# Kernel optimization log

Measured on AMD Instinct MI355X. Metric: run time of the kernel, lower is better.

The kernel has to match this reference:

```python
import jax, jax.numpy as jnp
import numpy as np

HIDDEN = 4096
NUM_BLOCKS = 8
BLOCK = HIDDEN // NUM_BLOCKS  # 512


def setup_inputs() -> dict:
    key = jax.random.key(0)
    k1, k2, k3, k4 = jax.random.split(key, 4)
    return {
        "weight": jax.random.normal(k1, (HIDDEN, HIDDEN), dtype=jnp.float32) * 0.02,
        "bias": jax.random.normal(k2, (HIDDEN,), dtype=jnp.float32) * 0.02,
        "x": jax.random.normal(k3, (4, 2048, HIDDEN), dtype=jnp.float32),
        "proj_R": jax.random.normal(k4, (NUM_BLOCKS, BLOCK, BLOCK), dtype=jnp.float32) * 0.02,
        "layer_idx": 0,
    }


def _cayley_batch(A):
    # Q = (I - S) @ inv(I + S + 1e-6*I), S = 0.5*(A - A^T), batched over blocks
    r = A.shape[-1]
    I = jnp.eye(r, dtype=A.dtype)
    S = 0.5 * (A - jnp.swapaxes(A, -2, -1))
    Minv = jnp.linalg.inv(I + S + 1e-6 * I)
    return jnp.einsum('bij,bjk->bik', I - S, Minv)


def reference(weight, bias, x, proj_R, layer_idx):
    Q = _cayley_batch(proj_R)                     # [nb, bs, bs], orthogonal blocks
    nb, bs, _ = Q.shape
    # block_diag(Q) @ weight == batched block-row matmul (off-diagonal blocks are zero)
    Wb = weight.reshape(nb, bs, weight.shape[1])  # [nb, bs, in]
    filt = jnp.einsum('bij,bjk->bik', Q, Wb).reshape(nb * bs, weight.shape[1])
    # F.linear(x, filt, bias)
    return jnp.einsum('bsi,oi->bso', x, filt) + bias
```

## Files before the change

### kernel.cpp

```cpp
#include <hip/hip_runtime.h>

typedef unsigned short u16;
typedef __attribute__((ext_vector_type(8))) short bf16x8;
typedef __attribute__((ext_vector_type(4))) float f32x4;
typedef __attribute__((ext_vector_type(8))) unsigned short u16x8;
typedef __attribute__((ext_vector_type(4))) unsigned short u16x4;

__device__ __forceinline__ u16 f2bf(float f){
  unsigned int u = __builtin_bit_cast(unsigned int, f);
  u += 0x7FFFu + ((u >> 16) & 1u);
  return (u16)(u >> 16);
}
__device__ __forceinline__ float bf2f(u16 h){
  unsigned int u = ((unsigned int)h) << 16;
  return __builtin_bit_cast(float, u);
}

__device__ __forceinline__ void load16(const u16* g, u16* s){
  __builtin_amdgcn_global_load_lds((const __attribute__((address_space(1))) unsigned int*)g,
                                   (__attribute__((address_space(3))) unsigned int*)s,
                                   16, 0, 0);
}

__global__ __launch_bounds__(256) void build_s(const float* __restrict__ R, u16* __restrict__ Sbf,
                                               u16* __restrict__ Dbf){
  int idx = blockIdx.x * 256 + threadIdx.x;
  int b = idx >> 18;
  int i = (idx >> 9) & 511;
  int j = idx & 511;
  float a  = R[idx];
  float at = R[(b << 18) + (j << 9) + i];
  float s = 0.5f * (a - at);
  Sbf[idx] = f2bf(s);
  Dbf[idx] = f2bf((i == j ? 2.000003f : 0.0f) - 2.000001f * s);
}

__global__ __launch_bounds__(256) void conv_bf16(const float* __restrict__ src, u16* __restrict__ dst){
  size_t i = (size_t)blockIdx.x * 256 + threadIdx.x;
  const float4* s = (const float4*)src + i * 2;
  float4 v0 = s[0], v1 = s[1];
  u16x8 o = { f2bf(v0.x), f2bf(v0.y), f2bf(v0.z), f2bf(v0.w),
              f2bf(v1.x), f2bf(v1.y), f2bf(v1.z), f2bf(v1.w) };
  *(u16x8*)(dst + i * 8) = o;
}

__global__ __launch_bounds__(256) void transpose_w(const float* __restrict__ W, u16* __restrict__ Wt){
  const int b = blockIdx.z;
  const int i0 = blockIdx.x << 5;
  const int j0 = blockIdx.y << 5;
  __shared__ float tile[32][33];
  const int t = threadIdx.x;
  const int r = t >> 3, c = (t & 7) << 2;
  float4 v = *(const float4*)&W[(size_t)((b << 9) + j0 + r) * 4096 + i0 + c];
  tile[r][c+0] = v.x; tile[r][c+1] = v.y; tile[r][c+2] = v.z; tile[r][c+3] = v.w;
  __syncthreads();
  u16x4 o = { f2bf(tile[c+0][r]), f2bf(tile[c+1][r]), f2bf(tile[c+2][r]), f2bf(tile[c+3][r]) };
  *(u16x4*)&Wt[((size_t)b << 21) + (size_t)(i0 + r) * 512 + j0 + c] = o;
}

template<int EPI>
__global__ __launch_bounds__(256) void gemm_bt(const u16* __restrict__ A, const u16* __restrict__ B,
                                               void* __restrict__ Cout, const void* __restrict__ aux,
                                               void* __restrict__ aux2,
                                               int M, int N, int K){
  const int bz = blockIdx.z;
  const u16* Ab = A + (size_t)bz * M * K;
  const u16* Bb = B + (size_t)bz * N * K;
  const int m0 = blockIdx.y << 7, n0 = blockIdx.x << 7;
  __shared__ __align__(16) u16 As[4096];
  __shared__ __align__(16) u16 Bs[4096];
  const int t = threadIdx.x;
  const int w = t >> 6, l = t & 63;
  const int wr = w >> 1, wc = w & 1;
  const int kofs = (l & 3) << 3;
  const int rA = l >> 2;
  const int aRd = ((wr << 6) + (l & 15)) * 32 + ((l >> 4) << 3);
  const int bRd = ((wc << 6) + (l & 15)) * 32 + ((l >> 4) << 3);
  f32x4 acc[4][4] = {};
  for (int k0 = 0; k0 < K; k0 += 32){
#pragma unroll
    for (int j = 0; j < 2; ++j){
      int rowBase = ((w << 1) + j) << 4;
      load16(&Ab[(size_t)(m0 + rowBase + rA) * K + k0 + kofs], &As[((w << 1) + j) << 9]);
      load16(&Bb[(size_t)(n0 + rowBase + rA) * K + k0 + kofs], &Bs[((w << 1) + j) << 9]);
    }
    __syncthreads();
    bf16x8 aF[4], bF[4];
#pragma unroll
    for (int mf = 0; mf < 4; ++mf) aF[mf] = *(const bf16x8*)&As[aRd + (mf << 9)];
#pragma unroll
    for (int nf = 0; nf < 4; ++nf) bF[nf] = *(const bf16x8*)&Bs[bRd + (nf << 9)];
#pragma unroll
    for (int mf = 0; mf < 4; ++mf)
#pragma unroll
      for (int nf = 0; nf < 4; ++nf)
        acc[mf][nf] = __builtin_amdgcn_mfma_f32_16x16x32_bf16(aF[mf], bF[nf], acc[mf][nf], 0, 0, 0);
    __syncthreads();
  }
#pragma unroll
  for (int mf = 0; mf < 4; ++mf){
#pragma unroll
    for (int nf = 0; nf < 4; ++nf){
      const int col = n0 + (wc << 6) + (nf << 4) + (l & 15);
#pragma unroll
      for (int q = 0; q < 4; ++q){
        const int row = m0 + (wr << 6) + (mf << 4) + ((l >> 4) << 2) + q;
        float v = acc[mf][nf][q];
        size_t gi = ((size_t)bz * M + row) * N + col;
        size_t g2 = (((size_t)bz * M + row) << 10) + col;
        if (EPI == 3){
          ((u16*)Cout)[gi] = f2bf((row == col ? 2.0f : 0.0f) - v);
        } else if (EPI == 6){
          ((u16*)Cout)[gi] = f2bf(bf2f(((const u16*)aux)[gi]) + v);
        } else if (EPI == 7){
          u16 o = f2bf(v);
          ((u16*)Cout)[gi] = o;
          u16* d = (u16*)const_cast<void*>(aux);
          d[g2] = o;
          d[g2 + 512] = o;
        } else if (EPI == 9){
          ((u16*)Cout)[gi] = f2bf(v - (row == col ? 1.0f : 0.0f));
        } else if (EPI == 10){
          ((u16*)Cout)[gi] = f2bf((row == col ? 1.0f : 0.0f) - v);
        } else {
          float p = v + (row == col ? 1.000002f : 0.0f);
          u16 ph = f2bf(p);
          ((u16*)Cout)[g2] = ph;
          ((u16*)Cout)[g2 + 512] = f2bf(p - bf2f(ph));
          const float beta = 0.8264463f;
          u16 x1 = f2bf((row == col ? 2.0f * beta : 0.0f) - beta * beta * p);
          ((u16*)const_cast<void*>(aux))[gi] = x1;
          ((u16*)aux2)[g2] = x1;
          ((u16*)aux2)[g2 + 512] = x1;
        }
      }
    }
  }
}

template<int EPI>
__global__ __launch_bounds__(512, 2) void gemm256(const u16* __restrict__ A, const u16* __restrict__ B,
                                                  void* __restrict__ Cout, const float* __restrict__ aux,
                                                  int M, int N, int K){
  __shared__ __align__(16) char lds[131072];
  const int bz = blockIdx.z;
  const char* Ab = (const char*)(A + (size_t)bz * M * K);
  const char* Bb = (const char*)(B + (size_t)bz * N * K);
  const int NB = N >> 8;
  const int nwg = gridDim.x;
  const int bid = blockIdx.x;
  const int swzb = (bid & 7) * (nwg >> 3) + (bid >> 3);
  const int m0 = (swzb / NB) << 8;
  const int n0 = (swzb % NB) << 8;
  const int tid = threadIdx.x;
  const int w = tid >> 6, l = tid & 63;
  const int wm = w >> 2, wn = w & 3;
  const size_t Kb = (size_t)K << 1;
  const int NT = K >> 6;
  const int sRow = tid >> 3;
  const int sCol = ((tid & 7) << 4) ^ ((sRow & 7) << 4);
  const int sDst = tid << 4;
  const char* aS = Ab + (size_t)(m0 + sRow) * Kb + sCol;
  const char* bS = Bb + (size_t)(n0 + sRow) * Kb + sCol;
  const int lrow = (l & 15) << 7;
  const int kq0 = (((l >> 4) << 4)) ^ ((l & 7) << 4);
  const int aOff = (wm << 14) + lrow;
  const int bOff = 32768 + ((wn >> 1) << 14) + ((wn & 1) << 13) + lrow;

#define STAGE_H(isB, h, tt) { \
    const int _lo = (((tt) & 1) << 16) + ((isB) << 15) + ((h) << 14); \
    const char* _s = ((isB) ? bS : aS) + ((size_t)((h) << 7)) * Kb + ((size_t)(tt) << 7); \
    load16((const u16*)_s, (u16*)(lds + _lo + sDst)); \
    load16((const u16*)(_s + (Kb << 6)), (u16*)(lds + _lo + 8192 + sDst)); }

#define RD_A(bufb, UQ) \
  _Pragma("unroll") for (int i2 = 0; i2 < 4; ++i2){ \
    aF[i2][0] = *(const bf16x8*)(lds + (bufb) + aOff + ((UQ) << 13) + (i2 << 11) + kq0); \
    aF[i2][1] = *(const bf16x8*)(lds + (bufb) + aOff + ((UQ) << 13) + (i2 << 11) + (kq0 ^ 64)); }

#define RD_B(bufb, VQ) \
  _Pragma("unroll") for (int j2 = 0; j2 < 2; ++j2){ \
    bF[VQ][j2][0] = *(const bf16x8*)(lds + (bufb) + bOff + ((VQ) << 12) + (j2 << 11) + kq0); \
    bF[VQ][j2][1] = *(const bf16x8*)(lds + (bufb) + bOff + ((VQ) << 12) + (j2 << 11) + (kq0 ^ 64)); }

#define MFMA16(UQ, VQ) \
    _Pragma("unroll") for (int i2 = 0; i2 < 4; ++i2) \
      _Pragma("unroll") for (int j2 = 0; j2 < 2; ++j2){ \
        acc[(UQ)*4+i2][(VQ)*2+j2] = __builtin_amdgcn_mfma_f32_16x16x32_bf16(aF[i2][0], bF[VQ][j2][0], acc[(UQ)*4+i2][(VQ)*2+j2], 0, 0, 0); \
        acc[(UQ)*4+i2][(VQ)*2+j2] = __builtin_amdgcn_mfma_f32_16x16x32_bf16(aF[i2][1], bF[VQ][j2][1], acc[(UQ)*4+i2][(VQ)*2+j2], 0, 0, 0); }

#define BAR asm volatile("s_barrier" ::: "memory");
#define VM0 asm volatile("s_waitcnt vmcnt(0)" ::: "memory");

  bf16x8 aF[4][2], bF[2][2][2];
  f32x4 acc[8][4] = {};

  STAGE_H(0,0,0) STAGE_H(1,0,0) STAGE_H(0,1,0) STAGE_H(1,1,0)
  VM0 BAR

#define KTILE(t, bufb) { \
    RD_A(bufb, 0) RD_B(bufb, 0) \
    if ((t) + 1 < NT) { STAGE_H(0,0,(t)+1) STAGE_H(1,0,(t)+1) } \
    MFMA16(0,0) \
    RD_B(bufb, 1) \
    if ((t) + 1 < NT) { STAGE_H(0,1,(t)+1) STAGE_H(1,1,(t)+1) } \
    MFMA16(0,1) \
    RD_A(bufb, 1) \
    MFMA16(1,1) \
    MFMA16(1,0) \
    __builtin_amdgcn_sched_barrier(0); \
    VM0 BAR }

#pragma unroll 1
  for (int tp = 0; tp < NT; tp += 2){
    KTILE(tp, 0)
    KTILE(tp+1, 65536)
  }
#undef KTILE
#undef STAGE_H
#undef RD_A
#undef RD_B
#undef MFMA16
#undef BAR
#undef VM0

#pragma unroll
  for (int mf = 0; mf < 8; ++mf){
#pragma unroll
    for (int nf = 0; nf < 4; ++nf){
      const int col = n0 + (wn << 6) + (nf << 4) + (l & 15);
#pragma unroll
      for (int q = 0; q < 4; ++q){
        const int row = m0 + (wm << 7) + (mf << 4) + ((l >> 4) << 2) + q;
        float v = acc[mf][nf][q];
        if (EPI == 0){
          ((float*)Cout)[(size_t)row * N + col] = v + aux[col];
        } else {
          ((u16*)Cout)[((size_t)bz * M + row) * N + col] = f2bf(v);
        }
      }
    }
  }
}

extern "C" void kernel_launch(void* const* d_in, const int* in_sizes, int n_in,
                              void* d_out, int out_size, void* d_ws, size_t ws_size,
                              hipStream_t stream){
  const float* W    = (const float*)d_in[0];
  const float* bias = (const float*)d_in[1];
  const float* x    = (const float*)d_in[2];
  const float* R    = (const float*)d_in[3];
  (void)in_sizes; (void)n_in; (void)out_size; (void)ws_size;

  char* ws = (char*)d_ws;
  const size_t MiB = (size_t)1 << 20;
  u16*   Sbf  = (u16*)(ws + 0 * MiB);
  u16*   Dbf  = (u16*)(ws + 4 * MiB);
  u16*   X1   = (u16*)(ws + 16 * MiB);
  u16*   Ybf  = (u16*)(ws + 20 * MiB);
  u16*   X2   = (u16*)(ws + 24 * MiB);
  u16*   Phl  = (u16*)(ws + 28 * MiB);
  u16*   X2d  = (u16*)(ws + 36 * MiB);
  u16*   X1d  = (u16*)(ws + 44 * MiB);
  u16*   Rbf  = X1;
  u16*   X3   = Ybf;
  u16*   G    = Sbf;
  u16*   Wt   = (u16*)(ws + 8 * MiB);
  u16*   filt = (u16*)(ws + 64 * MiB);
  u16*   xbf  = (u16*)(ws + 0 * MiB);

  const dim3 gNS(4, 4, 8);

  build_s<<<8192, 256, 0, stream>>>(R, Sbf, Dbf);
  gemm_bt<11><<<gNS, 256, 0, stream>>>(Sbf, Sbf, Phl, X1, X1d, 512, 512, 512);
  gemm_bt<3><<<gNS, 256, 0, stream>>>(Phl, X1d, Ybf, nullptr, nullptr, 512, 512, 1024);
  gemm_bt<7><<<gNS, 256, 0, stream>>>(X1, Ybf, X2, X2d, nullptr, 512, 512, 512);
  gemm_bt<10><<<gNS, 256, 0, stream>>>(Phl, X2d, Rbf, nullptr, nullptr, 512, 512, 1024);
  gemm_bt<6><<<gNS, 256, 0, stream>>>(X2, Rbf, X3, X2, nullptr, 512, 512, 512);
  gemm_bt<9><<<gNS, 256, 0, stream>>>(Dbf, X3, G, nullptr, nullptr, 512, 512, 512);
  transpose_w<<<dim3(128, 16, 8), 256, 0, stream>>>(W, Wt);
  gemm256<2><<<dim3(32, 1, 8), 512, 0, stream>>>(G, Wt, (void*)filt, nullptr, 512, 4096, 512);
  conv_bf16<<<16384, 256, 0, stream>>>(x, xbf);
  gemm256<0><<<dim3(512, 1, 1), 512, 0, stream>>>(xbf, filt, d_out, bias, 8192, 4096, 4096);
}
```

Before: 410.5 us.

## Use 4-wave 256x256 GEMM blocks with 128x128 per-wave tiles

Moves the main GEMM kernel from 8 waves (512 threads) to 4 waves (256 threads) per 256x256 output tile, so each wave now computes a 128x128 sub-tile with an 8x8 grid of 16x16 MFMA accumulators. The interleaved half-stage prefetch and MFMA schedule is replaced by a simpler order: issue all next-tile global-to-LDS loads, read all fragments, then run two 64-MFMA groups. The aim is more fragment reuse per LDS read and fewer waves contending for LDS bandwidth. In exchange, register use per thread roughly doubles (256 accumulator floats plus 32 fragment vectors), which can lower occupancy or spill, and there are fewer waves available to hide latency.

```diff
diff --git a/kernel.cpp b/kernel.cpp
--- a/kernel.cpp
+++ b/kernel.cpp
@@ -139,7 +139,7 @@
 }
 
 template<int EPI>
-__global__ __launch_bounds__(512, 2) void gemm256(const u16* __restrict__ A, const u16* __restrict__ B,
+__global__ __launch_bounds__(256, 1) void gemm256(const u16* __restrict__ A, const u16* __restrict__ B,
                                                   void* __restrict__ Cout, const float* __restrict__ aux,
                                                   int M, int N, int K){
   __shared__ __align__(16) char lds[131072];
@@ -154,7 +154,7 @@
   const int n0 = (swzb % NB) << 8;
   const int tid = threadIdx.x;
   const int w = tid >> 6, l = tid & 63;
-  const int wm = w >> 2, wn = w & 3;
+  const int wm = w >> 1, wn = w & 1;
   const size_t Kb = (size_t)K << 1;
   const int NT = K >> 6;
   const int sRow = tid >> 3;
@@ -162,52 +162,42 @@
   const int sDst = tid << 4;
   const char* aS = Ab + (size_t)(m0 + sRow) * Kb + sCol;
   const char* bS = Bb + (size_t)(n0 + sRow) * Kb + sCol;
-  const int lrow = (l & 15) << 7;
   const int kq0 = (((l >> 4) << 4)) ^ ((l & 7) << 4);
-  const int aOff = (wm << 14) + lrow;
-  const int bOff = 32768 + ((wn >> 1) << 14) + ((wn & 1) << 13) + lrow;
-
-#define STAGE_H(isB, h, tt) { \
-    const int _lo = (((tt) & 1) << 16) + ((isB) << 15) + ((h) << 14); \
-    const char* _s = ((isB) ? bS : aS) + ((size_t)((h) << 7)) * Kb + ((size_t)(tt) << 7); \
-    load16((const u16*)_s, (u16*)(lds + _lo + sDst)); \
-    load16((const u16*)(_s + (Kb << 6)), (u16*)(lds + _lo + 8192 + sDst)); }
-
-#define RD_A(bufb, UQ) \
-  _Pragma("unroll") for (int i2 = 0; i2 < 4; ++i2){ \
-    aF[i2][0] = *(const bf16x8*)(lds + (bufb) + aOff + ((UQ) << 13) + (i2 << 11) + kq0); \
-    aF[i2][1] = *(const bf16x8*)(lds + (bufb) + aOff + ((UQ) << 13) + (i2 << 11) + (kq0 ^ 64)); }
-
-#define RD_B(bufb, VQ) \
-  _Pragma("unroll") for (int j2 = 0; j2 < 2; ++j2){ \
-    bF[VQ][j2][0] = *(const bf16x8*)(lds + (bufb) + bOff + ((VQ) << 12) + (j2 << 11) + kq0); \
-    bF[VQ][j2][1] = *(const bf16x8*)(lds + (bufb) + bOff + ((VQ) << 12) + (j2 << 11) + (kq0 ^ 64)); }
-
-#define MFMA16(UQ, VQ) \
-    _Pragma("unroll") for (int i2 = 0; i2 < 4; ++i2) \
-      _Pragma("unroll") for (int j2 = 0; j2 < 2; ++j2){ \
-        acc[(UQ)*4+i2][(VQ)*2+j2] = __builtin_amdgcn_mfma_f32_16x16x32_bf16(aF[i2][0], bF[VQ][j2][0], acc[(UQ)*4+i2][(VQ)*2+j2], 0, 0, 0); \
-        acc[(UQ)*4+i2][(VQ)*2+j2] = __builtin_amdgcn_mfma_f32_16x16x32_bf16(aF[i2][1], bF[VQ][j2][1], acc[(UQ)*4+i2][(VQ)*2+j2], 0, 0, 0); }
+  const int aOff = (wm << 14) + ((l & 15) << 7);
+  const int bOff = 32768 + (wn << 14) + ((l & 15) << 7);
+
+#define STAGE8(isB, tt) { \
+    const int _bo = (((tt) & 1) << 16) + ((isB) << 15); \
+    const char* _s = ((isB) ? bS : aS) + ((size_t)(tt) << 7); \
+    _Pragma("unroll") for (int L = 0; L < 8; ++L) \
+      load16((const u16*)(_s + ((size_t)(L << 5)) * Kb), (u16*)(lds + _bo + (L << 12) + sDst)); }
+
+#define RD_A(dst, bufb, kx) \
+  _Pragma("unroll") for (int i = 0; i < 8; ++i) \
+    dst[i] = *(const bf16x8*)(lds + (bufb) + aOff + (i << 11) + (kq0 ^ (kx)));
+#define RD_B(dst, bufb, kx) \
+  _Pragma("unroll") for (int j = 0; j < 8; ++j) \
+    dst[j] = *(const bf16x8*)(lds + (bufb) + bOff + (j << 11) + (kq0 ^ (kx)));
+#define MFMA64(af, bf) \
+  _Pragma("unroll") for (int i = 0; i < 8; ++i) \
+    _Pragma("unroll") for (int j = 0; j < 8; ++j) \
+      acc[i][j] = __builtin_amdgcn_mfma_f32_16x16x32_bf16(af[i], bf[j], acc[i][j], 0, 0, 0);
 
 #define BAR asm volatile("s_barrier" ::: "memory");
 #define VM0 asm volatile("s_waitcnt vmcnt(0)" ::: "memory");
 
-  bf16x8 aF[4][2], bF[2][2][2];
-  f32x4 acc[8][4] = {};
-
-  STAGE_H(0,0,0) STAGE_H(1,0,0) STAGE_H(0,1,0) STAGE_H(1,1,0)
+  bf16x8 aF0[8], bF0[8], aF1[8], bF1[8];
+  f32x4 acc[8][8] = {};
+
+  STAGE8(0, 0) STAGE8(1, 0)
   VM0 BAR
 
 #define KTILE(t, bufb) { \
-    RD_A(bufb, 0) RD_B(bufb, 0) \
-    if ((t) + 1 < NT) { STAGE_H(0,0,(t)+1) STAGE_H(1,0,(t)+1) } \
-    MFMA16(0,0) \
-    RD_B(bufb, 1) \
-    if ((t) + 1 < NT) { STAGE_H(0,1,(t)+1) STAGE_H(1,1,(t)+1) } \
-    MFMA16(0,1) \
-    RD_A(bufb, 1) \
-    MFMA16(1,1) \
-    MFMA16(1,0) \
+    if ((t) + 1 < NT) { STAGE8(0, (t)+1) STAGE8(1, (t)+1) } \
+    RD_A(aF0, bufb, 0) RD_B(bF0, bufb, 0) \
+    RD_A(aF1, bufb, 64) RD_B(bF1, bufb, 64) \
+    MFMA64(aF0, bF0) \
+    MFMA64(aF1, bF1) \
     __builtin_amdgcn_sched_barrier(0); \
     VM0 BAR }
 
@@ -217,26 +207,26 @@
     KTILE(tp+1, 65536)
   }
 #undef KTILE
-#undef STAGE_H
+#undef STAGE8
 #undef RD_A
 #undef RD_B
-#undef MFMA16
+#undef MFMA64
 #undef BAR
 #undef VM0
 
 #pragma unroll
-  for (int mf = 0; mf < 8; ++mf){
-#pragma unroll
-    for (int nf = 0; nf < 4; ++nf){
-      const int col = n0 + (wn << 6) + (nf << 4) + (l & 15);
+  for (int i = 0; i < 8; ++i){
+    const int row = m0 + (wm << 7) + (i << 4) + ((l >> 4) << 2);
+#pragma unroll
+    for (int j = 0; j < 8; ++j){
+      const int col = n0 + (wn << 7) + (j << 4) + (l & 15);
 #pragma unroll
       for (int q = 0; q < 4; ++q){
-        const int row = m0 + (wm << 7) + (mf << 4) + ((l >> 4) << 2) + q;
-        float v = acc[mf][nf][q];
+        float v = acc[i][j][q];
         if (EPI == 0){
-          ((float*)Cout)[(size_t)row * N + col] = v + aux[col];
+          ((float*)Cout)[(size_t)(row + q) * N + col] = v + aux[col];
         } else {
-          ((u16*)Cout)[((size_t)bz * M + row) * N + col] = f2bf(v);
+          ((u16*)Cout)[((size_t)bz * M + row + q) * N + col] = f2bf(v);
         }
       }
     }
@@ -279,7 +269,7 @@
   gemm_bt<6><<<gNS, 256, 0, stream>>>(X2, Rbf, X3, X2, nullptr, 512, 512, 512);
   gemm_bt<9><<<gNS, 256, 0, stream>>>(Dbf, X3, G, nullptr, nullptr, 512, 512, 512);
   transpose_w<<<dim3(128, 16, 8), 256, 0, stream>>>(W, Wt);
-  gemm256<2><<<dim3(32, 1, 8), 512, 0, stream>>>(G, Wt, (void*)filt, nullptr, 512, 4096, 512);
+  gemm256<2><<<dim3(32, 1, 8), 256, 0, stream>>>(G, Wt, (void*)filt, nullptr, 512, 4096, 512);
   conv_bf16<<<16384, 256, 0, stream>>>(x, xbf);
-  gemm256<0><<<dim3(512, 1, 1), 512, 0, stream>>>(xbf, filt, d_out, bias, 8192, 4096, 4096);
-}
+  gemm256<0><<<dim3(512, 1, 1), 256, 0, stream>>>(xbf, filt, d_out, bias, 8192, 4096, 4096);
+}
```

New measurement: 555.8 us. +35.4%, slower.

## Shrink Newton-Schulz GEMM tiles to 128x64 with XOR-swizzled LDS layout

Applied to the files above, without the earlier changes.

The small batched 512x512 GEMMs used for the iterative matrix inverse now use 128x64 output tiles instead of 128x128, which doubles the grid from 128 to 256 workgroups to fill more compute units. Each wave now computes a 32x64 slab. The LDS staging layout changes to 64-byte rows with an XOR swizzle on the k-quarter to reduce bank conflicts on fragment reads. The trade-off is less data reuse per tile and more redundant A-tile loads.

```diff
diff --git a/kernel.cpp b/kernel.cpp
--- a/kernel.cpp
+++ b/kernel.cpp
@@ -59,52 +59,51 @@
 }
 
 template<int EPI>
-__global__ __launch_bounds__(256) void gemm_bt(const u16* __restrict__ A, const u16* __restrict__ B,
-                                               void* __restrict__ Cout, const void* __restrict__ aux,
+__global__ __launch_bounds__(256) void gemm_ns(const u16* __restrict__ A, const u16* __restrict__ B,
+                                               void* __restrict__ Cout, void* __restrict__ aux,
                                                void* __restrict__ aux2,
                                                int M, int N, int K){
   const int bz = blockIdx.z;
-  const u16* Ab = A + (size_t)bz * M * K;
-  const u16* Bb = B + (size_t)bz * N * K;
-  const int m0 = blockIdx.y << 7, n0 = blockIdx.x << 7;
-  __shared__ __align__(16) u16 As[4096];
-  __shared__ __align__(16) u16 Bs[4096];
+  const char* Ab = (const char*)(A + (size_t)bz * M * K);
+  const char* Bb = (const char*)(B + (size_t)bz * N * K);
+  const int m0 = blockIdx.y << 7, n0 = blockIdx.x << 6;
+  __shared__ __align__(16) char As[8192];
+  __shared__ __align__(16) char Bs[4096];
   const int t = threadIdx.x;
   const int w = t >> 6, l = t & 63;
-  const int wr = w >> 1, wc = w & 1;
-  const int kofs = (l & 3) << 3;
-  const int rA = l >> 2;
-  const int aRd = ((wr << 6) + (l & 15)) * 32 + ((l >> 4) << 3);
-  const int bRd = ((wc << 6) + (l & 15)) * 32 + ((l >> 4) << 3);
-  f32x4 acc[4][4] = {};
+  const size_t Kb = (size_t)K << 1;
+  const int sR = t >> 2;
+  const int sK = ((t ^ (t >> 2)) & 3) << 4;
+  const int kq = (((l >> 4) ^ l) & 3) << 4;
+  const int aRd = ((w << 5) + (l & 15)) * 64 + kq;
+  const int bRd = (l & 15) * 64 + kq;
+  f32x4 acc[2][4] = {};
   for (int k0 = 0; k0 < K; k0 += 32){
-#pragma unroll
-    for (int j = 0; j < 2; ++j){
-      int rowBase = ((w << 1) + j) << 4;
-      load16(&Ab[(size_t)(m0 + rowBase + rA) * K + k0 + kofs], &As[((w << 1) + j) << 9]);
-      load16(&Bb[(size_t)(n0 + rowBase + rA) * K + k0 + kofs], &Bs[((w << 1) + j) << 9]);
-    }
+    const size_t kb = (size_t)k0 << 1;
+    load16((const u16*)(Ab + (size_t)(m0 + sR) * Kb + kb + sK),      (u16*)(As + t * 16));
+    load16((const u16*)(Ab + (size_t)(m0 + 64 + sR) * Kb + kb + sK), (u16*)(As + 4096 + t * 16));
+    load16((const u16*)(Bb + (size_t)(n0 + sR) * Kb + kb + sK),      (u16*)(Bs + t * 16));
     __syncthreads();
-    bf16x8 aF[4], bF[4];
-#pragma unroll
-    for (int mf = 0; mf < 4; ++mf) aF[mf] = *(const bf16x8*)&As[aRd + (mf << 9)];
-#pragma unroll
-    for (int nf = 0; nf < 4; ++nf) bF[nf] = *(const bf16x8*)&Bs[bRd + (nf << 9)];
-#pragma unroll
-    for (int mf = 0; mf < 4; ++mf)
+    bf16x8 aF[2], bF[4];
+#pragma unroll
+    for (int mf = 0; mf < 2; ++mf) aF[mf] = *(const bf16x8*)(As + aRd + (mf << 10));
+#pragma unroll
+    for (int nf = 0; nf < 4; ++nf) bF[nf] = *(const bf16x8*)(Bs + bRd + (nf << 10));
+#pragma unroll
+    for (int mf = 0; mf < 2; ++mf)
 #pragma unroll
       for (int nf = 0; nf < 4; ++nf)
         acc[mf][nf] = __builtin_amdgcn_mfma_f32_16x16x32_bf16(aF[mf], bF[nf], acc[mf][nf], 0, 0, 0);
     __syncthreads();
   }
 #pragma unroll
-  for (int mf = 0; mf < 4; ++mf){
+  for (int mf = 0; mf < 2; ++mf){
 #pragma unroll
     for (int nf = 0; nf < 4; ++nf){
-      const int col = n0 + (wc << 6) + (nf << 4) + (l & 15);
+      const int col = n0 + (nf << 4) + (l & 15);
 #pragma unroll
       for (int q = 0; q < 4; ++q){
-        const int row = m0 + (wr << 6) + (mf << 4) + ((l >> 4) << 2) + q;
+        const int row = m0 + (w << 5) + (mf << 4) + ((l >> 4) << 2) + q;
         float v = acc[mf][nf][q];
         size_t gi = ((size_t)bz * M + row) * N + col;
         size_t g2 = (((size_t)bz * M + row) << 10) + col;
@@ -115,9 +114,8 @@
         } else if (EPI == 7){
           u16 o = f2bf(v);
           ((u16*)Cout)[gi] = o;
-          u16* d = (u16*)const_cast<void*>(aux);
-          d[g2] = o;
-          d[g2 + 512] = o;
+          ((u16*)aux)[g2] = o;
+          ((u16*)aux)[g2 + 512] = o;
         } else if (EPI == 9){
           ((u16*)Cout)[gi] = f2bf(v - (row == col ? 1.0f : 0.0f));
         } else if (EPI == 10){
@@ -129,7 +127,7 @@
           ((u16*)Cout)[g2 + 512] = f2bf(p - bf2f(ph));
           const float beta = 0.8264463f;
           u16 x1 = f2bf((row == col ? 2.0f * beta : 0.0f) - beta * beta * p);
-          ((u16*)const_cast<void*>(aux))[gi] = x1;
+          ((u16*)aux)[gi] = x1;
           ((u16*)aux2)[g2] = x1;
           ((u16*)aux2)[g2 + 512] = x1;
         }
@@ -269,15 +267,15 @@
   u16*   filt = (u16*)(ws + 64 * MiB);
   u16*   xbf  = (u16*)(ws + 0 * MiB);
 
-  const dim3 gNS(4, 4, 8);
+  const dim3 gNS(8, 4, 8);
 
   build_s<<<8192, 256, 0, stream>>>(R, Sbf, Dbf);
-  gemm_bt<11><<<gNS, 256, 0, stream>>>(Sbf, Sbf, Phl, X1, X1d, 512, 512, 512);
-  gemm_bt<3><<<gNS, 256, 0, stream>>>(Phl, X1d, Ybf, nullptr, nullptr, 512, 512, 1024);
-  gemm_bt<7><<<gNS, 256, 0, stream>>>(X1, Ybf, X2, X2d, nullptr, 512, 512, 512);
-  gemm_bt<10><<<gNS, 256, 0, stream>>>(Phl, X2d, Rbf, nullptr, nullptr, 512, 512, 1024);
-  gemm_bt<6><<<gNS, 256, 0, stream>>>(X2, Rbf, X3, X2, nullptr, 512, 512, 512);
-  gemm_bt<9><<<gNS, 256, 0, stream>>>(Dbf, X3, G, nullptr, nullptr, 512, 512, 512);
+  gemm_ns<11><<<gNS, 256, 0, stream>>>(Sbf, Sbf, Phl, X1, X1d, 512, 512, 512);
+  gemm_ns<3><<<gNS, 256, 0, stream>>>(Phl, X1d, Ybf, nullptr, nullptr, 512, 512, 1024);
+  gemm_ns<7><<<gNS, 256, 0, stream>>>(X1, Ybf, X2, X2d, nullptr, 512, 512, 512);
+  gemm_ns<10><<<gNS, 256, 0, stream>>>(Phl, X2d, Rbf, nullptr, nullptr, 512, 512, 1024);
+  gemm_ns<6><<<gNS, 256, 0, stream>>>(X2, Rbf, X3, X2, nullptr, 512, 512, 512);
+  gemm_ns<9><<<gNS, 256, 0, stream>>>(Dbf, X3, G, nullptr, nullptr, 512, 512, 512);
   transpose_w<<<dim3(128, 16, 8), 256, 0, stream>>>(W, Wt);
   gemm256<2><<<dim3(32, 1, 8), 512, 0, stream>>>(G, Wt, (void*)filt, nullptr, 512, 4096, 512);
   conv_bf16<<<16384, 256, 0, stream>>>(x, xbf);
```

Measured after the change: 388.2 us. 1.06x faster.
